# Performance work log

Measured on AMD Instinct MI355X. Metric: run time of the kernel, lower is better.

## Reference

```python
import jax, jax.numpy as jnp
import numpy as np

B, C, T, F = 8, 256, 256, 128
D, H, HEADS, K = 64, 128, 4, 8
I = D * K  # unfold channel dim = D*8


def _conv2d(x, w, b, stride=1, pad=0):
    y = jax.lax.conv_general_dilated(x, w, (stride, stride), [(pad, pad), (pad, pad)],
                                     dimension_numbers=('NCHW', 'OIHW', 'NCHW'))
    return y + b[None, :, None, None]


def _convT(x, w, b, strides):
    y = jax.lax.conv_transpose(x, w, strides, 'VALID', dimension_numbers=('NCHW', 'OIHW', 'NCHW'))
    return y + b[None, :, None, None]


def _sru_dir(x, Wx, bf, br, Whw):
    # x: (N, L, I). SRU: all matmuls precomputed, only elementwise recurrence in scan.
    u = jnp.einsum('nli,ih->nlh', x, Wx)  # (N, L, 3H)
    xt, fp, rp = jnp.split(u, 3, axis=-1)
    f = jax.nn.sigmoid(fp + bf)
    r = jax.nn.sigmoid(rp + br)
    xhw = jnp.einsum('nli,ih->nlh', x, Whw)  # highway projection (I != H)

    def step(c, inp):
        xt_t, f_t, r_t, xhw_t = inp
        c = f_t * c + (1.0 - f_t) * xt_t
        h = r_t * c + (1.0 - r_t) * xhw_t
        return c, h

    c0 = jnp.zeros((x.shape[0], bf.shape[-1]), x.dtype)
    seq = tuple(jnp.swapaxes(a, 0, 1) for a in (xt, f, r, xhw))  # (L, N, H)
    _, hs = jax.lax.scan(step, c0, seq)
    return jnp.swapaxes(hs, 0, 1)  # (N, L, H)


def _sru_bidir(x, Wx, bf, br, Whw):
    hf = _sru_dir(x, Wx[0], bf[0], br[0], Whw[0])
    hb = _sru_dir(x[:, ::-1], Wx[1], bf[1], br[1], Whw[1])[:, ::-1]
    return jnp.concatenate([hf, hb], axis=-1)  # (N, L, 2H)


def _unfold_last(x, k):
    # nn.Unfold(kernel=(1,k)) over last axis: (B,D,T,F) -> (B, D*k, T, F-k+1)
    L = x.shape[-1] - k + 1
    p = jnp.stack([x[..., i:i + L] for i in range(k)], axis=2)  # (B, D, k, T, L)
    b, d = x.shape[0], x.shape[1]
    return p.reshape(b, d * k, x.shape[2], L)


def _pathway(ag, Wx, bf, br, Whw, pw, pb, ctw, ctb):
    # unfold -> bidirectional SRU over last axis -> proj -> ConvTranspose2d(I->D, kernel (1,8))
    b, d, t, f = ag.shape
    L = f - K + 1
    u = _unfold_last(ag, K)                                  # (B, I, t, L)
    seq = u.transpose(0, 2, 3, 1).reshape(b * t, L, d * K)   # scan along unfolded axis
    h = _sru_bidir(seq, Wx, bf, br, Whw)                     # (b*t, L, 2H)
    z = h @ pw + pb                                          # (b*t, L, I)
    z = z.reshape(b, t, L, d * K).transpose(0, 3, 1, 2)      # (B, I, t, L)
    return _convT(z, ctw, ctb, (1, 1))                       # (B, D, t, f)


def _attention(x, qkv_w, qkv_b, ow, ob):
    b, d, t, f = x.shape
    n = t * f
    tok = x.reshape(b, d, n).transpose(0, 2, 1)  # (B, N, D)
    qkv = tok @ qkv_w + qkv_b
    q, k, v = jnp.split(qkv, 3, axis=-1)
    dh = d // HEADS
    sp = lambda a: a.reshape(b, n, HEADS, dh).transpose(0, 2, 1, 3)
    q, k, v = sp(q), sp(k), sp(v)
    s = jnp.einsum('bhnd,bhmd->bhnm', q, k) / jnp.sqrt(jnp.asarray(dh, x.dtype))
    a = jax.nn.softmax(s, axis=-1)
    o = jnp.einsum('bhnm,bhmd->bhnd', a, v).transpose(0, 2, 1, 3).reshape(b, n, d)
    o = o @ ow + ob
    return o.transpose(0, 2, 1).reshape(b, d, t, f)


def _forward(A, compress_w, compress_b, down_w0, down_b0, down_w1, down_b1,
             f_Wx, f_bf, f_br, f_Whw, f_proj_w, f_proj_b, f_ct_w, f_ct_b,
             t_Wx, t_bf, t_br, t_Whw, t_proj_w, t_proj_b, t_ct_w, t_ct_b,
             qkv_w, qkv_b, out_w, out_b, up_w0, up_b0, up_w1, up_b1, final_w, final_b):
    # Compressor: 1x1 conv C->D then 2 strided downsample units
    x0 = _conv2d(A, compress_w, compress_b)                              # (B,D,T,F)
    x1 = jax.nn.relu(_conv2d(x0, down_w0, down_b0, stride=2, pad=1))     # (B,D,T/2,F/2)
    x2 = jax.nn.relu(_conv2d(x1, down_w1, down_b1, stride=2, pad=1))     # (B,D,T/4,F/4)
    ag = x2
    # Dual path: frequency scan then time scan, with residuals as in _dual_path
    freq_out = _pathway(ag, f_Wx, f_bf, f_br, f_Whw, f_proj_w, f_proj_b, f_ct_w, f_ct_b) + ag
    agt = ag.transpose(0, 1, 3, 2)  # scan over time axis
    time_out = _pathway(agt, t_Wx, t_bf, t_br, t_Whw, t_proj_w, t_proj_b, t_ct_w, t_ct_b).transpose(0, 1, 3, 2) + freq_out
    # TF self-attention with residual
    dp = _attention(time_out, qkv_w, qkv_b, out_w, out_b) + time_out
    # U-Net style reconstruction with skips, project back to C
    y = _convT(dp, up_w0, up_b0, (2, 2)) + x1
    y = _convT(y, up_w1, up_b1, (2, 2)) + x0
    return _conv2d(y, final_w, final_b)                                  # (B,C,T,F)


def setup_inputs() -> dict:
    key = jax.random.key(0)
    ks = iter(jax.random.split(key, 64))

    def p(shape, scale=0.05):
        return jax.random.normal(next(ks), shape, dtype=jnp.float32) * scale

    inp = dict(
        A=jax.random.normal(next(ks), (B, C, T, F), dtype=jnp.float32),
        compress_w=p((D, C, 1, 1)), compress_b=p((D,)),
        down_w0=p((D, D, 3, 3)), down_b0=p((D,)),
        down_w1=p((D, D, 3, 3)), down_b1=p((D,)),
        f_Wx=p((2, I, 3 * H)), f_bf=p((2, H)), f_br=p((2, H)), f_Whw=p((2, I, H)),
        f_proj_w=p((2 * H, I)), f_proj_b=p((I,)), f_ct_w=p((D, I, 1, K)), f_ct_b=p((D,)),
        t_Wx=p((2, I, 3 * H)), t_bf=p((2, H)), t_br=p((2, H)), t_Whw=p((2, I, H)),
        t_proj_w=p((2 * H, I)), t_proj_b=p((I,)), t_ct_w=p((D, I, 1, K)), t_ct_b=p((D,)),
        qkv_w=p((D, 3 * D)), qkv_b=p((3 * D,)), out_w=p((D, D)), out_b=p((D,)),
        up_w0=p((D, D, 2, 2)), up_b0=p((D,)),
        up_w1=p((D, D, 2, 2)), up_b1=p((D,)),
        final_w=p((C, D, 1, 1)), final_b=p((C,)),
    )
    return inp


def reference(A, compress_w, compress_b, down_w0, down_b0, down_w1, down_b1,
              f_Wx, f_bf, f_br, f_Whw, f_proj_w, f_proj_b, f_ct_w, f_ct_b,
              t_Wx, t_bf, t_br, t_Whw, t_proj_w, t_proj_b, t_ct_w, t_ct_b,
              qkv_w, qkv_b, out_w, out_b, up_w0, up_b0, up_w1, up_b1, final_w, final_b):
    return _forward(A, compress_w, compress_b, down_w0, down_b0, down_w1, down_b1,
                    f_Wx, f_bf, f_br, f_Whw, f_proj_w, f_proj_b, f_ct_w, f_ct_b,
                    t_Wx, t_bf, t_br, t_Whw, t_proj_w, t_proj_b, t_ct_w, t_ct_b,
                    qkv_w, qkv_b, out_w, out_b, up_w0, up_b0, up_w1, up_b1, final_w, final_b)
```

## Files before the change

kernel.cpp:

```cpp
#include <hip/hip_runtime.h>

#define BB 8
#define CC 256
#define TT 256
#define FF 128
#define DD 64
#define HH 128
#define NHEADS 4
#define KK 8
#define II 512
#define T2 128
#define F2 64
#define T4 64
#define F4 32
#define P4 2048

#define LF 25
#define LT 57
#define MF (512*LF)
#define MT (256*LT)

typedef __attribute__((ext_vector_type(8))) short bf16x8;
typedef __attribute__((ext_vector_type(4))) float f32x4;

// ... 32 lines not shown
    if (bid < 64)        { int g = bid * 256 + tid; cw16[g] = f2b(cw[g]); return; }
    if (bid < 128)       { int g = (bid - 64) * 256 + tid; fw16[g] = f2b(fw[g]); return; }
    if (bid < 256) {
        const float* w = (bid < 192) ? upw0 : upw1;
        ushort* O = (bid < 192) ? WupT0 : WupT1;
        int g = ((bid - 128) & 63) * 256 + tid;
        int c = g & 63; int n = g >> 6;
        int parity = n >> 6, d = n & 63;
        O[g] = f2b(w[((d * 64 + c) * 2 + (1 - (parity >> 1))) * 2 + (1 - (parity & 1))]);
        return;
    }
    if (bid < 304) {
        int g = (bid - 256) * 256 + tid;
        int k = g & 63, n = g >> 6;
        qkvwT[g] = f2b(qkv_w[k * 192 + n]); return;
    }
    if (bid < 320) {
        int g = (bid - 304) * 256 + tid;
        int k = g & 63, n = g >> 6;
        owT[g] = f2b(ow[k * 64 + n]); return;
    }
    if (bid < 608) {
        const float* w = (bid < 464) ? dw0 : dw1;
        ushort* O = (bid < 464) ? WT9d0 : WT9d1;
        int g = ((bid - 320) % 144) * 256 + tid;
        int c = g & 63; int rest = g >> 6;
        int d = rest & 63; int tap = rest >> 6;
        O[g] = f2b(w[(d * 64 + c) * 9 + tap]); return;
    }
    if (bid < 1632) {
        const float* w = (bid < 1120) ? f_pw : t_pw;
        ushort* O = (bid < 1120) ? pwF16 : pwT16;
        int g = ((bid - 608) % 512) * 256 + tid;
        O[g] = f2b(w[g]); return;
    }
    if (bid < 3680) {
        const float* ctw = (bid < 2656) ? f_ctw : t_ctw;
        ushort* O = (bid < 2656) ? WctF : WctT_;
        int g = ((bid - 1632) % 1024) * 256 + tid;
        int k = g & 511; int n = g >> 9;
        int tap = n >> 6, d = n & 63;
        O[g] = f2b(ctw[((d * 512) + k) * 8 + tap]); return;
    }
    {
        const float* Wx  = (bid < 5728) ? f_Wx  : t_Wx;
        const float* Whw = (bid < 5728) ? f_Whw : t_Whw;
        ushort* O = (bid < 5728) ? WcatF : WcatTm;
        int g = ((bid - 3680) % 2048) * 256 + tid;
        int k = g & 511; int n = g >> 9;
        int dir = n >> 9; int c = n & 511;
        float v = (c < 384) ? Wx[(dir * 512 + k) * 384 + c]
                            : Whw[(dir * 512 + k) * 128 + (c - 384)];
        O[g] = f2b(v);
    }
}

__global__ __launch_bounds__(256) void w3_gemm_k(
    const ushort* __restrict__ pwA, const ushort* __restrict__ wctA,
    const ushort* __restrict__ pwB, const ushort* __restrict__ wctB,
    ushort* __restrict__ w3A, ushort* __restrict__ w3B)
{
    const int M = 256, K = 512;
    const ushort* A16  = blockIdx.z ? pwB  : pwA;
    const ushort* BT16 = blockIdx.z ? wctB : wctA;
    ushort* C16        = blockIdx.z ? w3B  : w3A;
    __shared__ ushort As[128][40];
    __shared__ ushort Bs[128][40];
    int m0 = blockIdx.y * 128, n0 = blockIdx.x * 128;
    int tid = threadIdx.x;
    int wave = tid >> 6, lane = tid & 63;
    int wm = (wave & 1) * 64, wn = (wave >> 1) * 64;
    int l15 = lane & 15, lhi = lane >> 4;
    f32x4 acc[4][4] = {};
    int rs = tid >> 2, qs = tid & 3;

    for (int k0 = 0; k0 < K; k0 += 32) {
        *(uint4*)&As[rs][qs * 8]      = *(const uint4*)(A16 + (long long)(m0 + rs) * K + k0 + qs * 8);
        *(uint4*)&As[rs + 64][qs * 8] = *(const uint4*)(A16 + (long long)(m0 + rs + 64) * K + k0 + qs * 8);
        *(uint4*)&Bs[rs][qs * 8]      = *(const uint4*)(BT16 + (long long)(n0 + rs) * K + k0 + qs * 8);
        *(uint4*)&Bs[rs + 64][qs * 8] = *(const uint4*)(BT16 + (long long)(n0 + rs + 64) * K + k0 + qs * 8);
        __syncthreads();
        bf16x8 af[4], bfr[4];
#pragma unroll
        for (int fr = 0; fr < 4; ++fr)
            af[fr] = *(const bf16x8*)&As[wm + fr * 16 + l15][lhi * 8];
#pragma unroll
        for (int fc = 0; fc < 4; ++fc)
            bfr[fc] = *(const bf16x8*)&Bs[wn + fc * 16 + l15][lhi * 8];
#pragma unroll
        for (int fr = 0; fr < 4; ++fr)
#pragma unroll
            for (int fc = 0; fc < 4; ++fc)
                acc[fr][fc] = __builtin_amdgcn_mfma_f32_16x16x32_bf16(af[fr], bfr[fc], acc[fr][fc], 0, 0, 0);
        __syncthreads();
    }
#pragma unroll
    for (int fr = 0; fr < 4; ++fr)
#pragma unroll
        for (int fc = 0; fc < 4; ++fc) {
            int col = n0 + wn + fc * 16 + l15;
#pragma unroll
            for (int r = 0; r < 4; ++r) {
                int row = m0 + wm + fr * 16 + lhi * 4 + r;
                C16[(long long)col * M + row] = f2b(acc[fr][fc][r]);
            }
        }
}

__global__ void bias3_red_k(const float* __restrict__ pbF, const float* __restrict__ ctwF,
                            const float* __restrict__ pbT, const float* __restrict__ ctwT,
                            float* __restrict__ b3F, float* __restrict__ b3T)
{
    int n = blockIdx.x; int path = blockIdx.y;
    const float* pb  = path ? pbT  : pbF;
    const float* ctw = path ? ctwT : ctwF;
    float* b3        = path ? b3T  : b3F;
    int d = n & 63, tap = n >> 6;
    int tid = threadIdx.x;
    float s = 0.f;
    for (int i = tid; i < 512; i += 256)
        s += pb[i] * ctw[(d * 512 + i) * 8 + tap];
    __shared__ float red[256];
    red[tid] = s; __syncthreads();
    for (int st = 128; st > 0; st >>= 1) {
        if (tid < st) red[tid] += red[tid + st];
        __syncthreads();
    }
    if (tid == 0) b3[n] = red[0];
}

__global__ void unfold_both_k(const float* __restrict__ ag,
                              ushort* __restrict__ uF, ushort* __restrict__ uT)
{
    long long gid = (long long)blockIdx.x * blockDim.x + threadIdx.x;
    if (gid < (long long)MF * II) {
        int ch = (int)(gid & 511); int row = (int)(gid >> 9);
        int b = row / (T4 * LF); int rem = row - b * (T4 * LF);
        int t = rem / LF; int l = rem - t * LF;
        int d = ch >> 3, i = ch & 7;
        uF[gid] = f2b(ag[((long long)((b * DD + d) * T4 + t)) * F4 + l + i]);
    } else {
        long long g2 = gid - (long long)MF * II;
        int ch = (int)(g2 & 511); int row = (int)(g2 >> 9);
        int b = row / (F4 * LT); int rem = row - b * (F4 * LT);
        int tt = rem / LT; int l = rem - tt * LT;
        int d = ch >> 3, i = ch & 7;
        uT[g2] = f2b(ag[((long long)((b * DD + d) * T4 + (l + i))) * F4 + tt]);
    }
}

__global__ __launch_bounds__(256) void gates_fused_k(
    const ushort* __restrict__ uF, const ushort* __restrict__ uT,
    const ushort* __restrict__ WF, const ushort* __restrict__ WTm,
    ushort* __restrict__ GxtF, ushort* __restrict__ GxhF,
    ushort* __restrict__ GfF, ushort* __restrict__ GrF,
    ushort* __restrict__ GxtT, ushort* __restrict__ GxhT,
    ushort* __restrict__ GfT, ushort* __restrict__ GrT,
    const float* __restrict__ f_bf, const float* __restrict__ f_br,
    const float* __restrict__ t_bf, const float* __restrict__ t_br)
{
    __shared__ ushort As[128][40];
    __shared__ ushort Bs[128][40];
    const int K = 512;
    int by = blockIdx.y;
    bool tp = by >= 100;
    const ushort* A16 = tp ? uT : uF;
    const ushort* WT  = tp ? WTm : WF;
    ushort* Gxt = tp ? GxtT : GxtF;
    ushort* Gxh = tp ? GxhT : GxhF;
    ushort* Gf = tp ? GfT : GfF;
    ushort* Gr = tp ? GrT : GrF;
    const float* bfw = tp ? t_bf : f_bf;
    const float* brw = tp ? t_br : f_br;
    int m0 = (tp ? by - 100 : by) * 128;
    int n0 = blockIdx.x * 128;
    int tid = threadIdx.x, wave = tid >> 6, lane = tid & 63;
    int wm = (wave & 1) * 64, wn = (wave >> 1) * 64;
    int l15 = lane & 15, lhi = lane >> 4;
    f32x4 acc[4][4] = {};
    int rs = tid >> 2, qs = tid & 3;

    for (int k0 = 0; k0 < K; k0 += 32) {
        *(uint4*)&As[rs][qs * 8]      = *(const uint4*)(A16 + (long long)(m0 + rs) * K + k0 + qs * 8);
        *(uint4*)&As[rs + 64][qs * 8] = *(const uint4*)(A16 + (long long)(m0 + rs + 64) * K + k0 + qs * 8);
        *(uint4*)&Bs[rs][qs * 8]      = *(const uint4*)(WT + (long long)(n0 + rs) * K + k0 + qs * 8);
        *(uint4*)&Bs[rs + 64][qs * 8] = *(const uint4*)(WT + (long long)(n0 + rs + 64) * K + k0 + qs * 8);
        __syncthreads();
        bf16x8 af[4], bfr[4];
#pragma unroll
        for (int fr = 0; fr < 4; ++fr)
            af[fr] = *(const bf16x8*)&As[wm + fr * 16 + l15][lhi * 8];
#pragma unroll
        for (int fc = 0; fc < 4; ++fc)
            bfr[fc] = *(const bf16x8*)&Bs[wn + fc * 16 + l15][lhi * 8];
#pragma unroll
        for (int fr = 0; fr < 4; ++fr)
#pragma unroll
            for (int fc = 0; fc < 4; ++fc)
                acc[fr][fc] = __builtin_amdgcn_mfma_f32_16x16x32_bf16(af[fr], bfr[fc], acc[fr][fc], 0, 0, 0);
        __syncthreads();
    }
#pragma unroll
    for (int fc = 0; fc < 4; ++fc) {
        int col = n0 + wn + fc * 16 + l15;
        int dir = col >> 9, c = col & 511;
        int cls = c >> 7, h = c & 127;
        int dh = dir * 128 + h;
#pragma unroll
        for (int fr = 0; fr < 4; ++fr) {
#pragma unroll
            for (int r = 0; r < 4; ++r) {
                int row = m0 + wm + fr * 16 + lhi * 4 + r;
                long long idx = (long long)row * 256 + dh;
                float v = acc[fr][fc][r];
                if (cls == 0)      Gxt[idx] = f2b(v);
                else if (cls == 3) Gxh[idx] = f2b(v);
                else if (cls == 1) Gf[idx] = f2b(1.f / (1.f + __expf(-(v + bfw[dh]))));
                else               Gr[idx] = f2b(1.f / (1.f + __expf(-(v + brw[dh]))));
            }
        }
    }
}

__global__ void sru_scan_both_k(
    const ushort* __restrict__ GxtF, const ushort* __restrict__ GxhF,
    const ushort* __restrict__ GfF, const ushort* __restrict__ GrF,
    ushort* __restrict__ hF,
    const ushort* __restrict__ GxtT, const ushort* __restrict__ GxhT,
    const ushort* __restrict__ GfT, const ushort* __restrict__ GrT,
    ushort* __restrict__ hT)
{
    int gid = blockIdx.x * blockDim.x + threadIdx.x;
    const ushort *Gxt, *Gxh, *Gf, *Gr; ushort* hout; int L;
    if (gid < 512 * 256) {
        Gxt = GxtF; Gxh = GxhF; Gf = GfF; Gr = GrF; hout = hF; L = LF;
    } else {
        gid -= 512 * 256;
        Gxt = GxtT; Gxh = GxhT; Gf = GfT; Gr = GrT; hout = hT; L = LT;
    }
    int h = gid & 127; int dir = (gid >> 7) & 1; int n = gid >> 8;
    int dh = dir * 128 + h;
    float c = 0.f;
    for (int s = 0; s < L; ++s) {
        int l = dir ? (L - 1 - s) : s;
        long long off = (long long)(n * L + l) * 256 + dh;
        float xt = b2f(Gxt[off]), xh = b2f(Gxh[off]);
        float f = b2f(Gf[off]);
        float r = b2f(Gr[off]);
        c = f * c + (1.f - f) * xt;
        float hv = r * c + (1.f - r) * xh;
        hout[off] = f2b(hv);
    }
}

__global__ __launch_bounds__(256) void gemmW_both_k(
    const ushort* __restrict__ hF, const ushort* __restrict__ W3F,
    ushort* __restrict__ YF, const float* __restrict__ b3F,
    const ushort* __restrict__ hT, const ushort* __restrict__ W3T,
    ushort* __restrict__ YT, const float* __restrict__ b3T)
{
    __shared__ ushort As[128][40];
    __shared__ ushort Bs[128][40];
    const int N = 512, K = 256;
    int by = blockIdx.y;
    bool tp = by >= 100;
    const ushort* A16 = tp ? hT : hF;
    const ushort* WT  = tp ? W3T : W3F;
    ushort* C16       = tp ? YT : YF;
    const float* bias = tp ? b3T : b3F;
    int m0 = (tp ? by - 100 : by) * 128;
    int n0 = blockIdx.x * 128;
    int tid = threadIdx.x, wave = tid >> 6, lane = tid & 63;
    int wm = (wave & 1) * 64, wn = (wave >> 1) * 64;
    int l15 = lane & 15, lhi = lane >> 4;
    f32x4 acc[4][4] = {};
    int rs = tid >> 2, qs = tid & 3;

    for (int k0 = 0; k0 < K; k0 += 32) {
        *(uint4*)&As[rs][qs * 8]      = *(const uint4*)(A16 + (long long)(m0 + rs) * K + k0 + qs * 8);
        *(uint4*)&As[rs + 64][qs * 8] = *(const uint4*)(A16 + (long long)(m0 + rs + 64) * K + k0 + qs * 8);
        *(uint4*)&Bs[rs][qs * 8]      = *(const uint4*)(WT + (long long)(n0 + rs) * K + k0 + qs * 8);
        *(uint4*)&Bs[rs + 64][qs * 8] = *(const uint4*)(WT + (long long)(n0 + rs + 64) * K + k0 + qs * 8);
        __syncthreads();
        bf16x8 af[4], bfr[4];
#pragma unroll
        for (int fr = 0; fr < 4; ++fr)
            af[fr] = *(const bf16x8*)&As[wm + fr * 16 + l15][lhi * 8];
#pragma unroll
        for (int fc = 0; fc < 4; ++fc)
            bfr[fc] = *(const bf16x8*)&Bs[wn + fc * 16 + l15][lhi * 8];
#pragma unroll
        for (int fr = 0; fr < 4; ++fr)
#pragma unroll
            for (int fc = 0; fc < 4; ++fc)
                acc[fr][fc] = __builtin_amdgcn_mfma_f32_16x16x32_bf16(af[fr], bfr[fc], acc[fr][fc], 0, 0, 0);
        __syncthreads();
    }
#pragma unroll
    for (int fc = 0; fc < 4; ++fc) {
        int col = n0 + wn + fc * 16 + l15;
        float bv = bias[col];
#pragma unroll
        for (int fr = 0; fr < 4; ++fr) {
#pragma unroll
            for (int r = 0; r < 4; ++r) {
                int row = m0 + wm + fr * 16 + lhi * 4 + r;
                C16[(long long)row * N + col] = f2b(acc[fr][fc][r] + bv);
            }
        }
    }
}

__global__ void dual_reduce_k(const ushort* __restrict__ YF, const ushort* __restrict__ YT,
                              const float* __restrict__ f_ctb, const float* __restrict__ t_ctb,
                              const float* __restrict__ ag, float* __restrict__ tout)
{
    int gid = blockIdx.x * blockDim.x + threadIdx.x;
    int d = gid & 63; int rest = gid >> 6;
    int f = rest & 31; rest >>= 5;
    int t = rest & 63; int b = rest >> 6;
    float v = f_ctb[d] + t_ctb[d];
    long long ybF = ((long long)(b * 64 + t)) * LF;
    long long ybT = ((long long)(b * 32 + f)) * LT;
#pragma unroll
    for (int tap = 0; tap < 8; ++tap) {
        int lf = f + tap - 7;
        if (lf >= 0 && lf < LF) v += b2f(YF[(ybF + lf) * 512 + tap * 64 + d]);
        int lt = t + tap - 7;
        if (lt >= 0 && lt < LT) v += b2f(YT[(ybT + lt) * 512 + tap * 64 + d]);
    }
    long long oi = (((long long)(b * 64 + d)) * 64 + t) * 32 + f;
    tout[oi] = v + ag[oi];
}

template<int BN>
__global__ __launch_bounds__(256) void mfma_nchw_k(
    const float* __restrict__ X, const ushort* __restrict__ WT,
    const float* __restrict__ bias, float* __restrict__ Y,
    int P, int N, int K)
{
    constexpr int FC = BN / 32;
    __shared__ ushort As[128][40];
    int p0 = blockIdx.x * 128;
    int n0 = blockIdx.y * BN;
    int b  = blockIdx.z;
    int tid = threadIdx.x, wave = tid >> 6, lane = tid & 63;
    int l15 = lane & 15, lhi = lane >> 4;
    int wm = (wave & 1) * 64, wn = (wave >> 1) * (BN / 2);
    f32x4 acc[4][FC] = {};
    const float* Xb = X + (long long)b * K * P;
    int kk_s = tid >> 3, pq_s = tid & 7;

    for (int k0 = 0; k0 < K; k0 += 32) {
        const float* xr = Xb + (long long)(k0 + kk_s) * P + p0;
#pragma unroll
        for (int j = 0; j < 4; ++j) {
            float4 v = *(const float4*)(xr + j * 32 + pq_s * 4);
            int pp = j * 32 + pq_s * 4;
            As[pp][kk_s]     = f2b(v.x);
            As[pp + 1][kk_s] = f2b(v.y);
            As[pp + 2][kk_s] = f2b(v.z);
            As[pp + 3][kk_s] = f2b(v.w);
        }
        __syncthreads();
        bf16x8 af[4], bfr[FC];
#pragma unroll
        for (int fr = 0; fr < 4; ++fr)
            af[fr] = *(const bf16x8*)&As[wm + fr * 16 + l15][lhi * 8];
#pragma unroll
        for (int fc = 0; fc < FC; ++fc)
            bfr[fc] = *(const bf16x8*)(WT + (long long)(n0 + wn + fc * 16 + l15) * K + k0 + lhi * 8);
#pragma unroll
        for (int fr = 0; fr < 4; ++fr)
#pragma unroll
            for (int fc = 0; fc < FC; ++fc)
                acc[fr][fc] = __builtin_amdgcn_mfma_f32_16x16x32_bf16(af[fr], bfr[fc], acc[fr][fc], 0, 0, 0);
        __syncthreads();
    }
#pragma unroll
    for (int fc = 0; fc < FC; ++fc) {
        int n = n0 + wn + fc * 16 + l15;
        float bv = bias[n];
        float* yr = Y + ((long long)(b * N + n)) * P + p0 + wm + lhi * 4;
#pragma unroll
        for (int fr = 0; fr < 4; ++fr) {
            float4 o;
            o.x = acc[fr][fc][0] + bv;
            o.y = acc[fr][fc][1] + bv;
            o.z = acc[fr][fc][2] + bv;
            o.w = acc[fr][fc][3] + bv;
            *(float4*)(yr + fr * 16) = o;
        }
    }
}

__global__ __launch_bounds__(256) void mfma_nchw16_k(
    const ushort* __restrict__ X, const ushort* __restrict__ WT,
    const float* __restrict__ bias, float* __restrict__ Y,
    int P, int N, int K)
{
    constexpr int BN = 128, FC = 4;
    __shared__ ushort As[128][40];
    int p0 = blockIdx.x * 128;
    int n0 = blockIdx.y * BN;
    int b  = blockIdx.z;
    int tid = threadIdx.x, wave = tid >> 6, lane = tid & 63;
    int l15 = lane & 15, lhi = lane >> 4;
    int wm = (wave & 1) * 64, wn = (wave >> 1) * (BN / 2);
    f32x4 acc[4][FC] = {};
    const ushort* Xb = X + (long long)b * K * P;
    int kk_s = tid >> 3, pq_s = tid & 7;

    for (int k0 = 0; k0 < K; k0 += 32) {
        const ushort* xr = Xb + (long long)(k0 + kk_s) * P + p0 + pq_s * 16;
#pragma unroll
        for (int j = 0; j < 2; ++j) {
            uint4 v = *(const uint4*)(xr + j * 8);
            const ushort* e = (const ushort*)&v;
            int pp = pq_s * 16 + j * 8;
#pragma unroll
            for (int t = 0; t < 8; ++t) As[pp + t][kk_s] = e[t];
        }
        __syncthreads();
        bf16x8 af[4], bfr[FC];
#pragma unroll
        for (int fr = 0; fr < 4; ++fr)
            af[fr] = *(const bf16x8*)&As[wm + fr * 16 + l15][lhi * 8];
#pragma unroll
        for (int fc = 0; fc < FC; ++fc)
            bfr[fc] = *(const bf16x8*)(WT + (long long)(n0 + wn + fc * 16 + l15) * K + k0 + lhi * 8);
#pragma unroll
        for (int fr = 0; fr < 4; ++fr)
#pragma unroll
            for (int fc = 0; fc < FC; ++fc)
                acc[fr][fc] = __builtin_amdgcn_mfma_f32_16x16x32_bf16(af[fr], bfr[fc], acc[fr][fc], 0, 0, 0);
        __syncthreads();
    }
#pragma unroll
    for (int fc = 0; fc < FC; ++fc) {
        int n = n0 + wn + fc * 16 + l15;
        float bv = bias[n];
        float* yr = Y + ((long long)(b * N + n)) * P + p0 + wm + lhi * 4;
#pragma unroll
        for (int fr = 0; fr < 4; ++fr) {
            float4 o;
            o.x = acc[fr][fc][0] + bv;
            o.y = acc[fr][fc][1] + bv;
            o.z = acc[fr][fc][2] + bv;
            o.w = acc[fr][fc][3] + bv;
            *(float4*)(yr + fr * 16) = o;
        }
    }
}

__global__ __launch_bounds__(256) void down_mfma_k(
    const float* __restrict__ in, const ushort* __restrict__ WT9,
    const float* __restrict__ bias, float* __restrict__ out,
    int Hi, int Wi)
{
    __shared__ ushort Is[289][64];
    int Ho = Hi >> 1, Wo = Wi >> 1;
    int ntx = Wo >> 3, nty = Ho >> 3;
    int tx = blockIdx.x % ntx; int rest = blockIdx.x / ntx;
    int ty = rest % nty; int b = rest / nty;
    int oy0 = ty * 8, ox0 = tx * 8;
    int iy0 = oy0 * 2 - 1, ix0 = ox0 * 2 - 1;
    int tid = threadIdx.x, wave = tid >> 6, lane = tid & 63;
    int l15 = lane & 15, lhi = lane >> 4;
    int wm = (wave & 1) * 32, wn = (wave >> 1) * 32;

    const float* ib = in + (long long)b * 64 * Hi * Wi;
    for (int i = tid; i < 289 * 64; i += 256) {
        int c = i / 289; int sp = i - c * 289;
        int r = sp / 17; int s = sp - r * 17;
        int iy = iy0 + r, ix = ix0 + s;
        float v = 0.f;
        if (iy >= 0 && iy < Hi && ix >= 0 && ix < Wi)
            v = ib[(long long)c * Hi * Wi + (long long)iy * Wi + ix];
        Is[sp][c ^ ((sp & 7) << 3)] = f2b(v);
    }
    __syncthreads();

    f32x4 acc[2][2] = {};
#pragma unroll
    for (int tap = 0; tap < 9; ++tap) {
        int kh = tap / 3, kw = tap - kh * 3;
#pragma unroll
        for (int half = 0; half < 2; ++half) {
            int c0 = half * 32 + lhi * 8;
            bf16x8 af[2], bw[2];
#pragma unroll
            for (int fr = 0; fr < 2; ++fr) {
                int p = wm + fr * 16 + l15;
                int sp = (2 * (p >> 3) + kh) * 17 + 2 * (p & 7) + kw;
                af[fr] = *(const bf16x8*)&Is[sp][c0 ^ ((sp & 7) << 3)];
            }
#pragma unroll
            for (int fc = 0; fc < 2; ++fc) {
                int d = wn + fc * 16 + l15;
                bw[fc] = *(const bf16x8*)(WT9 + (tap * 64 + d) * 64 + c0);
            }
#pragma unroll
            for (int fr = 0; fr < 2; ++fr)
#pragma unroll
                for (int fc = 0; fc < 2; ++fc)
                    acc[fr][fc] = __builtin_amdgcn_mfma_f32_16x16x32_bf16(af[fr], bw[fc], acc[fr][fc], 0, 0, 0);
        }
    }
#pragma unroll
    for (int fc = 0; fc < 2; ++fc) {
        int d = wn + fc * 16 + l15;
        float bv = bias[d];
        long long obase = ((long long)(b * 64 + d)) * Ho * Wo;
#pragma unroll
        for (int fr = 0; fr < 2; ++fr) {
#pragma unroll
            for (int r = 0; r < 4; ++r) {
                int p = wm + fr * 16 + lhi * 4 + r;
                int py = p >> 3, px = p & 7;
                out[obase + (long long)(oy0 + py) * Wo + ox0 + px] =
                    fmaxf(acc[fr][fc][r] + bv, 0.f);
            }
        }
    }
}

template<int OUT16>
__global__ __launch_bounds__(256) void up_mfma_k(
    const float* __restrict__ in, const ushort* __restrict__ WT,
    const float* __restrict__ bias, const float* __restrict__ resid,
    float* __restrict__ out, ushort* __restrict__ o16, int P, int wsh)
{
    __shared__ ushort As[128][72];
    int p0 = blockIdx.x * 128;
    int n0 = blockIdx.y * 128;
    int b  = blockIdx.z;
    int tid = threadIdx.x, wave = tid >> 6, lane = tid & 63;
    int l15 = lane & 15, lhi = lane >> 4;
    int wm = (wave & 1) * 64, wn = (wave >> 1) * 64;
    int Wi = 1 << wsh;
    int Ho = ((P >> wsh) << 1), Wo = Wi << 1;

    int kk_s = tid >> 3, pq_s = tid & 7;
#pragma unroll
    for (int h = 0; h < 2; ++h) {
        int k = h * 32 + kk_s;
        const float* xr = in + ((long long)(b * 64 + k)) * P + p0 + pq_s * 16;
#pragma unroll
        for (int j = 0; j < 4; ++j) {
            float4 v = *(const float4*)(xr + j * 4);
            int pp = pq_s * 16 + j * 4;
            As[pp][k]     = f2b(v.x);
            As[pp + 1][k] = f2b(v.y);
            As[pp + 2][k] = f2b(v.z);
            As[pp + 3][k] = f2b(v.w);
        }
    }
    __syncthreads();

    f32x4 acc[4][4] = {};
#pragma unroll
    for (int c = 0; c < 2; ++c) {
        bf16x8 af[4], bfr[4];
#pragma unroll
        for (int fr = 0; fr < 4; ++fr)
            af[fr] = *(const bf16x8*)&As[wm + fr * 16 + l15][c * 32 + lhi * 8];
#pragma unroll
        for (int fc = 0; fc < 4; ++fc)
            bfr[fc] = *(const bf16x8*)(WT + (long long)(n0 + wn + fc * 16 + l15) * 64 + c * 32 + lhi * 8);
#pragma unroll
        for (int fr = 0; fr < 4; ++fr)
#pragma unroll
            for (int fc = 0; fc < 4; ++fc)
                acc[fr][fc] = __builtin_amdgcn_mfma_f32_16x16x32_bf16(af[fr], bfr[fc], acc[fr][fc], 0, 0, 0);
    }

#pragma unroll
    for (int fc = 0; fc < 4; ++fc) {
        int n = n0 + wn + fc * 16 + l15;
        int parity = n >> 6, d = n & 63;
        int py = parity >> 1, px = parity & 1;
        float bv = bias[d];
        const long long obase = ((long long)(b * 64 + d)) * Ho * Wo;
#pragma unroll
        for (int fr = 0; fr < 4; ++fr) {
#pragma unroll
            for (int r = 0; r < 4; ++r) {
                int p = p0 + wm + fr * 16 + lhi * 4 + r;
                int iy = p >> wsh, ix = p & (Wi - 1);
                long long oi = obase + (long long)(2 * iy + py) * Wo + 2 * ix + px;
                float v = acc[fr][fc][r] + bv + resid[oi];
                if (OUT16) o16[oi] = f2b(v);
                else       out[oi] = v;
            }
        }
    }
}

__global__ __launch_bounds__(256) void mfma_qkv_k(
    const float* __restrict__ X, const ushort* __restrict__ WT,
    const float* __restrict__ bias, ushort* __restrict__ C16)
{
    __shared__ ushort As[128][72];
    int p0 = blockIdx.x * 128;
    int b  = blockIdx.z;
    int tid = threadIdx.x, wave = tid >> 6, lane = tid & 63;
    int l15 = lane & 15, lhi = lane >> 4;
    int wm = (wave & 1) * 64, wn = (wave >> 1) * 96;

    int kk_s = tid >> 3, pq_s = tid & 7;
#pragma unroll
    for (int h = 0; h < 2; ++h) {
        int k = h * 32 + kk_s;
        const float* xr = X + ((long long)(b * 64 + k)) * P4 + p0 + pq_s * 16;
#pragma unroll
        for (int j = 0; j < 4; ++j) {
            float4 v = *(const float4*)(xr + j * 4);
            int pp = pq_s * 16 + j * 4;
            As[pp][k]     = f2b(v.x);
            As[pp + 1][k] = f2b(v.y);
            As[pp + 2][k] = f2b(v.z);
            As[pp + 3][k] = f2b(v.w);
        }
    }
    __syncthreads();

    f32x4 acc[4][6] = {};
#pragma unroll
    for (int c = 0; c < 2; ++c) {
        bf16x8 af[4], bfr[6];
#pragma unroll
        for (int fr = 0; fr < 4; ++fr)
            af[fr] = *(const bf16x8*)&As[wm + fr * 16 + l15][c * 32 + lhi * 8];
#pragma unroll
        for (int fc = 0; fc < 6; ++fc)
            bfr[fc] = *(const bf16x8*)(WT + (long long)(wn + fc * 16 + l15) * 64 + c * 32 + lhi * 8);
#pragma unroll
        for (int fr = 0; fr < 4; ++fr)
#pragma unroll
            for (int fc = 0; fc < 6; ++fc)
                acc[fr][fc] = __builtin_amdgcn_mfma_f32_16x16x32_bf16(af[fr], bfr[fc], acc[fr][fc], 0, 0, 0);
    }
#pragma unroll
    for (int fc = 0; fc < 6; ++fc) {
        int n = wn + fc * 16 + l15;
        float bv = bias[n];
#pragma unroll
        for (int fr = 0; fr < 4; ++fr)
#pragma unroll
            for (int r = 0; r < 4; ++r) {
                int p = p0 + wm + fr * 16 + lhi * 4 + r;
                C16[((long long)(b * P4 + p)) * 192 + n] = f2b(acc[fr][fc][r] + bv);
            }
    }
}

__global__ __launch_bounds__(256) void mfma_attnout_k(
    const float* __restrict__ A, const ushort* __restrict__ owT,
    const float* __restrict__ ob, const float* __restrict__ resid,
    float* __restrict__ dp)
{
    __shared__ ushort As[128][72];
    int p0 = blockIdx.x * 128;
    int b  = blockIdx.z;
    int tid = threadIdx.x, wave = tid >> 6, lane = tid & 63;
    int l15 = lane & 15, lhi = lane >> 4;
    int wm = (wave & 1) * 64, wn = (wave >> 1) * 32;

    int rs = tid >> 2, qs = tid & 3;
#pragma unroll
    for (int h = 0; h < 2; ++h) {
        int row = h * 64 + rs;
        const float* ar = A + ((long long)(b * P4 + p0 + row)) * 64 + qs * 16;
#pragma unroll
        for (int j = 0; j < 4; ++j) {
            float4 v = *(const float4*)(ar + j * 4);
            int c = qs * 16 + j * 4;
            *(unsigned*)&As[row][c]     = cvtpk_bf16(v.x, v.y);
            *(unsigned*)&As[row][c + 2] = cvtpk_bf16(v.z, v.w);
        }
    }
    __syncthreads();

    f32x4 acc[4][2] = {};
#pragma unroll
    for (int c = 0; c < 2; ++c) {
        bf16x8 af[4], bfr[2];
#pragma unroll
        for (int fr = 0; fr < 4; ++fr)
            af[fr] = *(const bf16x8*)&As[wm + fr * 16 + l15][c * 32 + lhi * 8];
#pragma unroll
        for (int fc = 0; fc < 2; ++fc)
            bfr[fc] = *(const bf16x8*)(owT + (long long)(wn + fc * 16 + l15) * 64 + c * 32 + lhi * 8);
#pragma unroll
        for (int fr = 0; fr < 4; ++fr)
#pragma unroll
            for (int fc = 0; fc < 2; ++fc)
                acc[fr][fc] = __builtin_amdgcn_mfma_f32_16x16x32_bf16(af[fr], bfr[fc], acc[fr][fc], 0, 0, 0);
    }
#pragma unroll
    for (int fc = 0; fc < 2; ++fc) {
        int n = wn + fc * 16 + l15;
        float bv = ob[n];
        long long base = ((long long)(b * 64 + n)) * P4;
#pragma unroll
        for (int fr = 0; fr < 4; ++fr) {
            int p = p0 + wm + fr * 16 + lhi * 4;
            float4 rv = *(const float4*)(resid + base + p);
            float4 o;
            o.x = acc[fr][fc][0] + bv + rv.x;
            o.y = acc[fr][fc][1] + bv + rv.y;
            o.z = acc[fr][fc][2] + bv + rv.z;
            o.w = acc[fr][fc][3] + bv + rv.w;
            *(float4*)(dp + base + p) = o;
        }
    }
}

__global__ __launch_bounds__(256) void attn_mfma_k(const ushort* __restrict__ qkv,
                                                   float* __restrict__ out)
{
    __shared__ ushort Qs[128][40];
    __shared__ ushort Ks[64][40];
    __shared__ ushort VsT[16][72];
    __shared__ ushort Ps[128][72];
    int qt = blockIdx.x, h = blockIdx.y, b = blockIdx.z;
    int tid = threadIdx.x, wave = tid >> 6, lane = tid & 63;
    int l15 = lane & 15, lhi = lane >> 4;
    int q0 = wave * 32;

    for (int i = tid; i < 1024; i += 256) {
        int row = i >> 3, c = i & 7;
        *(unsigned*)&Qs[row][16 + c * 2] = 0u;
    }
    for (int i = tid; i < 512; i += 256) {
        int row = i >> 3, c = i & 7;
        *(unsigned*)&Ks[row][16 + c * 2] = 0u;
    }
    {
        const ushort* qp = qkv + ((long long)(b * P4 + qt * 128)) * 192 + h * 16;
        for (int i = tid; i < 2048; i += 256) {
            int row = i >> 4, d = i & 15;
            Qs[row][d] = f2b(b2f(qp[row * 192 + d]) * 0.25f);
        }
    }
    __syncthreads();

    float mmax[2] = {-1e30f, -1e30f};
    float lsum[2] = {0.f, 0.f};
    f32x4 oacc[2] = {};

    for (int k0 = 0; k0 < P4; k0 += 64) {
        const ushort* kp = qkv + ((long long)(b * P4 + k0)) * 192 + 64 + h * 16;
        for (int i = tid; i < 1024; i += 256) {
            int key = i >> 4, d = i & 15;
            Ks[key][d]  = kp[key * 192 + d];
            VsT[d][key] = kp[key * 192 + 64 + d];
        }
        __syncthreads();

        bf16x8 bq[2];
        bq[0] = *(const bf16x8*)&Qs[q0 + l15][lhi * 8];
        bq[1] = *(const bf16x8*)&Qs[q0 + 16 + l15][lhi * 8];
        f32x4 s[4][2];
#pragma unroll
        for (int fr = 0; fr < 4; ++fr) {
            bf16x8 ak = *(const bf16x8*)&Ks[fr * 16 + l15][lhi * 8];
            f32x4 z = {};
            s[fr][0] = __builtin_amdgcn_mfma_f32_16x16x32_bf16(ak, bq[0], z, 0, 0, 0);
            s[fr][1] = __builtin_amdgcn_mfma_f32_16x16x32_bf16(ak, bq[1], z, 0, 0, 0);
        }
#pragma unroll
        for (int fc = 0; fc < 2; ++fc) {
            float m = s[0][fc][0];
#pragma unroll
            for (int fr = 0; fr < 4; ++fr)
#pragma unroll
                for (int r = 0; r < 4; ++r) m = fmaxf(m, s[fr][fc][r]);
            m = fmaxf(m, __shfl_xor(m, 16));
            m = fmaxf(m, __shfl_xor(m, 32));
            float nm = fmaxf(mmax[fc], m);
            float corr = __expf(mmax[fc] - nm);
            mmax[fc] = nm;
            float ps = 0.f;
#pragma unroll
            for (int fr = 0; fr < 4; ++fr)
#pragma unroll
                for (int r = 0; r < 4; ++r) {
                    float p = __expf(s[fr][fc][r] - nm);
                    s[fr][fc][r] = p;
                    ps += p;
                }
            lsum[fc] = lsum[fc] * corr + ps;
#pragma unroll
            for (int r = 0; r < 4; ++r) oacc[fc][r] *= corr;
        }
#pragma unroll
        for (int fc = 0; fc < 2; ++fc)
#pragma unroll
            for (int fr = 0; fr < 4; ++fr) {
                uint2 pk;
                pk.x = cvtpk_bf16(s[fr][fc][0], s[fr][fc][1]);
                pk.y = cvtpk_bf16(s[fr][fc][2], s[fr][fc][3]);
                *(uint2*)&Ps[q0 + fc * 16 + l15][fr * 16 + lhi * 4] = pk;
            }
#pragma unroll
        for (int ks = 0; ks < 2; ++ks) {
            bf16x8 av = *(const bf16x8*)&VsT[l15][ks * 32 + lhi * 8];
#pragma unroll
            for (int fc = 0; fc < 2; ++fc) {
                bf16x8 bp = *(const bf16x8*)&Ps[q0 + fc * 16 + l15][ks * 32 + lhi * 8];
                oacc[fc] = __builtin_amdgcn_mfma_f32_16x16x32_bf16(av, bp, oacc[fc], 0, 0, 0);
            }
        }
        __syncthreads();
    }
#pragma unroll
    for (int fc = 0; fc < 2; ++fc) {
        float L = lsum[fc];
        L += __shfl_xor(L, 16);
        L += __shfl_xor(L, 32);
        float inv = 1.f / L;
        int q = qt * 128 + q0 + fc * 16 + l15;
        float* op = out + ((long long)(b * P4 + q)) * 64 + h * 16 + lhi * 4;
#pragma unroll
        for (int r = 0; r < 4; ++r) op[r] = oacc[fc][r] * inv;
    }
}

extern "C" void kernel_launch(void* const* d_in, const int* in_sizes, int n_in,
                              void* d_out, int out_size, void* d_ws, size_t ws_size,
                              hipStream_t stream)
{
    const float* A_in  = (const float*)d_in[0];
    const float* cw    = (const float*)d_in[1];
    const float* cb    = (const float*)d_in[2];
    const float* dw0   = (const float*)d_in[3];
    const float* db0   = (const float*)d_in[4];
    const float* dw1   = (const float*)d_in[5];
    const float* db1   = (const float*)d_in[6];
    const float* f_Wx  = (const float*)d_in[7];
    const float* f_bf  = (const float*)d_in[8];
    const float* f_br  = (const float*)d_in[9];
    const float* f_Whw = (const float*)d_in[10];
    const float* f_pw  = (const float*)d_in[11];
    const float* f_pb  = (const float*)d_in[12];
    const float* f_ctw = (const float*)d_in[13];
    const float* f_ctb = (const float*)d_in[14];
    const float* t_Wx  = (const float*)d_in[15];
    const float* t_bf  = (const float*)d_in[16];
    const float* t_br  = (const float*)d_in[17];
    const float* t_Whw = (const float*)d_in[18];
    const float* t_pw  = (const float*)d_in[19];
    const float* t_pb  = (const float*)d_in[20];
    const float* t_ctw = (const float*)d_in[21];
    const float* t_ctb = (const float*)d_in[22];
    const float* qkv_w = (const float*)d_in[23];
    const float* qkv_b = (const float*)d_in[24];
    const float* ow    = (const float*)d_in[25];
    const float* ob    = (const float*)d_in[26];
    const float* upw0  = (const float*)d_in[27];
    const float* upb0  = (const float*)d_in[28];
    const float* upw1  = (const float*)d_in[29];
    const float* upb1  = (const float*)d_in[30];
    const float* fw    = (const float*)d_in[31];
    const float* fb    = (const float*)d_in[32];

    float* ws  = (float*)d_ws;
    float* out = (float*)d_out;

    float* ag    = ws + 0;
    float* x1    = ws + 1048576;
    float* uFf   = ws + 5242880;
    float* uTf   = ws + 8519680;
    float* GxtF  = ws + 12255232;
    float* GxhF  = ws + 15532032;
    float* GxtT  = ws + 18808832;
    float* GxhT  = ws + 22544384;
    float* GfFf  = ws + 26279936;
    float* GrFf  = ws + 27918336;
    float* GfTf  = ws + 29556736;
    float* GrTf  = ws + 31424512;
    float* hFf   = ws + 33292288;
    float* hTf   = ws + 34930688;
    float* YF16f = ws + 5242880;
    float* YT16f = ws + 8519680;
    float* y016f = ws + 19267584;
    float* y1    = ws + 12255232;
    float* pwFf  = ws + 36798464;
    float* pwTf  = ws + 36864000;
    float* w3Ff  = ws + 36929536;
    float* w3Tf  = ws + 36995072;
    float* b3Ff  = ws + 37060608;
    float* b3Tf  = ws + 37061120;
    float* wctFf = ws + 37061632;
    float* wctTf = ws + 37192704;
    float* wcaFf = ws + 37323776;
    float* wcaTf = ws + 37585920;
    float* cw16f = ws + 37848064;
    float* fw16f = ws + 37856256;
    float* wup0f = ws + 37864448;
    float* wup1f = ws + 37872640;
    float* qkvwf = ws + 37880832;
    float* owtf  = ws + 37886976;
    float* wdw0f = ws + 37889024;
    float* wdw1f = ws + 37907456;
    float* tout  = ws + 37925888;
    float* qkvbf = ws + 38974464;
    float* attnO = ws + 40547328;
    float* dp    = ws + 41595904;

    ushort* uF     = (ushort*)uFf;
    ushort* uT     = (ushort*)uTf;
    ushort* GxtF16 = (ushort*)GxtF;
    ushort* GxhF16 = (ushort*)GxhF;
    ushort* GxtT16 = (ushort*)GxtT;
    ushort* GxhT16 = (ushort*)GxhT;
    ushort* GfF    = (ushort*)GfFf;
    ushort* GrF    = (ushort*)GrFf;
    ushort* GfT    = (ushort*)GfTf;
    ushort* GrT    = (ushort*)GrTf;
    ushort* hF     = (ushort*)hFf;
    ushort* hT     = (ushort*)hTf;
    ushort* YF16   = (ushort*)YF16f;
    ushort* YT16   = (ushort*)YT16f;
    ushort* y016   = (ushort*)y016f;
    ushort* pwF16  = (ushort*)pwFf;
    ushort* pwT16  = (ushort*)pwTf;
    ushort* W3F    = (ushort*)w3Ff;
    ushort* W3T_   = (ushort*)w3Tf;
    ushort* WctF   = (ushort*)wctFf;
    ushort* WctT_  = (ushort*)wctTf;
    ushort* WcatF  = (ushort*)wcaFf;
    ushort* WcatTm = (ushort*)wcaTf;
    ushort* qkv16  = (ushort*)qkvbf;
    ushort* cw16   = (ushort*)cw16f;
    ushort* fw16   = (ushort*)fw16f;
    ushort* WupT0  = (ushort*)wup0f;
    ushort* WupT1  = (ushort*)wup1f;
    ushort* qkvwT  = (ushort*)qkvwf;
    ushort* owT    = (ushort*)owtf;
    ushort* WT9d0  = (ushort*)wdw0f;
    ushort* WT9d1  = (ushort*)wdw1f;
    float*  x0     = out;

    dim3 blk(256);

    pack_all_k<<<dim3(7776), blk, 0, stream>>>(
        cw, fw, upw0, upw1, qkv_w, ow, dw0, dw1, f_pw, t_pw, f_ctw, t_ctw,
        f_Wx, f_Whw, t_Wx, t_Whw,
        cw16, fw16, WupT0, WupT1, qkvwT, owT, WT9d0, WT9d1,
        pwF16, pwT16, WctF, WctT_, WcatF, WcatTm);
    w3_gemm_k<<<dim3(4, 2, 2), blk, 0, stream>>>(pwF16, WctF, pwT16, WctT_, W3F, W3T_);
    bias3_red_k<<<dim3(512, 2), blk, 0, stream>>>(f_pb, f_ctw, t_pb, t_ctw, b3Ff, b3Tf);

    mfma_nchw_k<64><<<dim3(256, 1, 8), blk, 0, stream>>>(A_in, cw16, cb, x0, 32768, 64, 256);

    down_mfma_k<<<dim3(1024), blk, 0, stream>>>(x0, WT9d0, db0, x1, TT, FF);
    down_mfma_k<<<dim3(256), blk, 0, stream>>>(x1, WT9d1, db1, ag, T2, F2);

    unfold_both_k<<<dim3(54784), blk, 0, stream>>>(ag, uF, uT);
    gates_fused_k<<<dim3(8, 214), blk, 0, stream>>>(uF, uT, WcatF, WcatTm,
        GxtF16, GxhF16, GfF, GrF, GxtT16, GxhT16, GfT, GrT, f_bf, f_br, t_bf, t_br);
    sru_scan_both_k<<<dim3(768), blk, 0, stream>>>(GxtF16, GxhF16, GfF, GrF, hF,
                                                   GxtT16, GxhT16, GfT, GrT, hT);
    gemmW_both_k<<<dim3(4, 214), blk, 0, stream>>>(hF, W3F, YF16, b3Ff,
                                                   hT, W3T_, YT16, b3Tf);
    dual_reduce_k<<<dim3(8192), blk, 0, stream>>>(YF16, YT16, f_ctb, t_ctb, ag, tout);

    mfma_qkv_k<<<dim3(16, 1, 8), blk, 0, stream>>>(tout, qkvwT, qkv_b, qkv16);
    attn_mfma_k<<<dim3(16, NHEADS, BB), blk, 0, stream>>>(qkv16, attnO);
    mfma_attnout_k<<<dim3(16, 1, 8), blk, 0, stream>>>(attnO, owT, ob, tout, dp);

    up_mfma_k<0><<<dim3(16, 2, 8), blk, 0, stream>>>(dp, WupT0, upb0, x1, y1, nullptr, 2048, 5);
    up_mfma_k<1><<<dim3(64, 2, 8), blk, 0, stream>>>(y1, WupT1, upb1, x0, nullptr, y016, 8192, 6);

    mfma_nchw16_k<<<dim3(256, 2, 8), blk, 0, stream>>>(y016, fw16, fb, out, 32768, 256, 64);
}
```

Before: 680.2 us.

## Store encoder activations in bf16 and keep SRU xt/highway gates in fp32

The compress conv output and the first downsample output are now stored as bf16 and reused as bf16 residuals in the upsampling path, which halves their read/write traffic. The SRU candidate and highway projections are instead written as fp32 rather than bf16, presumably for accuracy, which doubles that traffic. The workspace is re-laid out with aliased buffers to fit the new sizes. The change trades activation bandwidth against precision in the residual path.

```diff
diff --git a/kernel.cpp b/kernel.cpp
--- a/kernel.cpp
+++ b/kernel.cpp
@@ -208,9 +208,9 @@
 __global__ __launch_bounds__(256) void gates_fused_k(
     const ushort* __restrict__ uF, const ushort* __restrict__ uT,
     const ushort* __restrict__ WF, const ushort* __restrict__ WTm,
-    ushort* __restrict__ GxtF, ushort* __restrict__ GxhF,
+    float* __restrict__ GxtF, float* __restrict__ GxhF,
     ushort* __restrict__ GfF, ushort* __restrict__ GrF,
-    ushort* __restrict__ GxtT, ushort* __restrict__ GxhT,
+    float* __restrict__ GxtT, float* __restrict__ GxhT,
     ushort* __restrict__ GfT, ushort* __restrict__ GrT,
     const float* __restrict__ f_bf, const float* __restrict__ f_br,
     const float* __restrict__ t_bf, const float* __restrict__ t_br)
@@ -222,8 +222,8 @@
     bool tp = by >= 100;
     const ushort* A16 = tp ? uT : uF;
     const ushort* WT  = tp ? WTm : WF;
-    ushort* Gxt = tp ? GxtT : GxtF;
-    ushort* Gxh = tp ? GxhT : GxhF;
+    float* Gxt = tp ? GxtT : GxtF;
+    float* Gxh = tp ? GxhT : GxhF;
     ushort* Gf = tp ? GfT : GfF;
     ushort* Gr = tp ? GrT : GrF;
     const float* bfw = tp ? t_bf : f_bf;
@@ -269,8 +269,8 @@
                 int row = m0 + wm + fr * 16 + lhi * 4 + r;
                 long long idx = (long long)row * 256 + dh;
                 float v = acc[fr][fc][r];
-                if (cls == 0)      Gxt[idx] = f2b(v);
-                else if (cls == 3) Gxh[idx] = f2b(v);
+                if (cls == 0)      Gxt[idx] = v;
+                else if (cls == 3) Gxh[idx] = v;
                 else if (cls == 1) Gf[idx] = f2b(1.f / (1.f + __expf(-(v + bfw[dh]))));
                 else               Gr[idx] = f2b(1.f / (1.f + __expf(-(v + brw[dh]))));
             }
@@ -279,15 +279,15 @@
 }
 
 __global__ void sru_scan_both_k(
-    const ushort* __restrict__ GxtF, const ushort* __restrict__ GxhF,
+    const float* __restrict__ GxtF, const float* __restrict__ GxhF,
     const ushort* __restrict__ GfF, const ushort* __restrict__ GrF,
     ushort* __restrict__ hF,
-    const ushort* __restrict__ GxtT, const ushort* __restrict__ GxhT,
+    const float* __restrict__ GxtT, const float* __restrict__ GxhT,
     const ushort* __restrict__ GfT, const ushort* __restrict__ GrT,
     ushort* __restrict__ hT)
 {
     int gid = blockIdx.x * blockDim.x + threadIdx.x;
-    const ushort *Gxt, *Gxh, *Gf, *Gr; ushort* hout; int L;
+    const float *Gxt, *Gxh; const ushort *Gf, *Gr; ushort* hout; int L;
     if (gid < 512 * 256) {
         Gxt = GxtF; Gxh = GxhF; Gf = GfF; Gr = GrF; hout = hF; L = LF;
     } else {
@@ -300,7 +300,7 @@
     for (int s = 0; s < L; ++s) {
         int l = dir ? (L - 1 - s) : s;
         long long off = (long long)(n * L + l) * 256 + dh;
-        float xt = b2f(Gxt[off]), xh = b2f(Gxh[off]);
+        float xt = Gxt[off], xh = Gxh[off];
         float f = b2f(Gf[off]);
         float r = b2f(Gr[off]);
         c = f * c + (1.f - f) * xt;
@@ -389,20 +389,19 @@
     tout[oi] = v + ag[oi];
 }
 
-template<int BN>
-__global__ __launch_bounds__(256) void mfma_nchw_k(
+__global__ __launch_bounds__(256) void mfma_nchw_o16_k(
     const float* __restrict__ X, const ushort* __restrict__ WT,
-    const float* __restrict__ bias, float* __restrict__ Y,
+    const float* __restrict__ bias, ushort* __restrict__ Y16,
     int P, int N, int K)
 {
-    constexpr int FC = BN / 32;
+    constexpr int FC = 2;
     __shared__ ushort As[128][40];
     int p0 = blockIdx.x * 128;
-    int n0 = blockIdx.y * BN;
+    int n0 = 0;
     int b  = blockIdx.z;
     int tid = threadIdx.x, wave = tid >> 6, lane = tid & 63;
     int l15 = lane & 15, lhi = lane >> 4;
-    int wm = (wave & 1) * 64, wn = (wave >> 1) * (BN / 2);
+    int wm = (wave & 1) * 64, wn = (wave >> 1) * 32;
     f32x4 acc[4][FC] = {};
     const float* Xb = X + (long long)b * K * P;
     int kk_s = tid >> 3, pq_s = tid & 7;
@@ -437,15 +436,13 @@
     for (int fc = 0; fc < FC; ++fc) {
         int n = n0 + wn + fc * 16 + l15;
         float bv = bias[n];
-        float* yr = Y + ((long long)(b * N + n)) * P + p0 + wm + lhi * 4;
+        ushort* yr = Y16 + ((long long)(b * N + n)) * P + p0 + wm + lhi * 4;
 #pragma unroll
         for (int fr = 0; fr < 4; ++fr) {
-            float4 o;
-            o.x = acc[fr][fc][0] + bv;
-            o.y = acc[fr][fc][1] + bv;
-            o.z = acc[fr][fc][2] + bv;
-            o.w = acc[fr][fc][3] + bv;
-            *(float4*)(yr + fr * 16) = o;
+            uint2 o;
+            o.x = cvtpk_bf16(acc[fr][fc][0] + bv, acc[fr][fc][1] + bv);
+            o.y = cvtpk_bf16(acc[fr][fc][2] + bv, acc[fr][fc][3] + bv);
+            *(uint2*)(yr + fr * 16) = o;
         }
     }
 }
@@ -509,10 +506,11 @@
     }
 }
 
+template<int OUT16>
 __global__ __launch_bounds__(256) void down_mfma_k(
-    const float* __restrict__ in, const ushort* __restrict__ WT9,
+    const ushort* __restrict__ in, const ushort* __restrict__ WT9,
     const float* __restrict__ bias, float* __restrict__ out,
-    int Hi, int Wi)
+    ushort* __restrict__ o16, int Hi, int Wi)
 {
     __shared__ ushort Is[289][64];
     int Ho = Hi >> 1, Wo = Wi >> 1;
@@ -525,15 +523,15 @@
     int l15 = lane & 15, lhi = lane >> 4;
     int wm = (wave & 1) * 32, wn = (wave >> 1) * 32;
 
-    const float* ib = in + (long long)b * 64 * Hi * Wi;
+    const ushort* ib = in + (long long)b * 64 * Hi * Wi;
     for (int i = tid; i < 289 * 64; i += 256) {
         int c = i / 289; int sp = i - c * 289;
         int r = sp / 17; int s = sp - r * 17;
         int iy = iy0 + r, ix = ix0 + s;
-        float v = 0.f;
+        ushort v = 0;
         if (iy >= 0 && iy < Hi && ix >= 0 && ix < Wi)
             v = ib[(long long)c * Hi * Wi + (long long)iy * Wi + ix];
-        Is[sp][c ^ ((sp & 7) << 3)] = f2b(v);
+        Is[sp][c ^ ((sp & 7) << 3)] = v;
     }
     __syncthreads();
 
@@ -574,8 +572,10 @@
             for (int r = 0; r < 4; ++r) {
                 int p = wm + fr * 16 + lhi * 4 + r;
                 int py = p >> 3, px = p & 7;
-                out[obase + (long long)(oy0 + py) * Wo + ox0 + px] =
-                    fmaxf(acc[fr][fc][r] + bv, 0.f);
+                long long oi = obase + (long long)(oy0 + py) * Wo + ox0 + px;
+                float v = fmaxf(acc[fr][fc][r] + bv, 0.f);
+                if (OUT16) o16[oi] = f2b(v);
+                else       out[oi] = v;
             }
         }
     }
@@ -584,7 +584,7 @@
 template<int OUT16>
 __global__ __launch_bounds__(256) void up_mfma_k(
     const float* __restrict__ in, const ushort* __restrict__ WT,
-    const float* __restrict__ bias, const float* __restrict__ resid,
+    const float* __restrict__ bias, const ushort* __restrict__ resid16,
     float* __restrict__ out, ushort* __restrict__ o16, int P, int wsh)
 {
     __shared__ ushort As[128][72];
@@ -645,7 +645,7 @@
                 int p = p0 + wm + fr * 16 + lhi * 4 + r;
                 int iy = p >> wsh, ix = p & (Wi - 1);
                 long long oi = obase + (long long)(2 * iy + py) * Wo + 2 * ix + px;
-                float v = acc[fr][fc][r] + bv + resid[oi];
+                float v = acc[fr][fc][r] + bv + b2f(resid16[oi]);
                 if (OUT16) o16[oi] = f2b(v);
                 else       out[oi] = v;
             }
@@ -926,52 +926,51 @@
     float* out = (float*)d_out;
 
     float* ag    = ws + 0;
-    float* x1    = ws + 1048576;
-    float* uFf   = ws + 5242880;
-    float* uTf   = ws + 8519680;
-    float* GxtF  = ws + 12255232;
-    float* GxhF  = ws + 15532032;
-    float* GxtT  = ws + 18808832;
-    float* GxhT  = ws + 22544384;
-    float* GfFf  = ws + 26279936;
-    float* GrFf  = ws + 27918336;
-    float* GfTf  = ws + 29556736;
-    float* GrTf  = ws + 31424512;
-    float* hFf   = ws + 33292288;
-    float* hTf   = ws + 34930688;
-    float* YF16f = ws + 5242880;
-    float* YT16f = ws + 8519680;
-    float* y016f = ws + 19267584;
-    float* y1    = ws + 12255232;
-    float* pwFf  = ws + 36798464;
-    float* pwTf  = ws + 36864000;
-    float* w3Ff  = ws + 36929536;
-    float* w3Tf  = ws + 36995072;
-    float* b3Ff  = ws + 37060608;
-    float* b3Tf  = ws + 37061120;
-    float* wctFf = ws + 37061632;
-    float* wctTf = ws + 37192704;
-    float* wcaFf = ws + 37323776;
-    float* wcaTf = ws + 37585920;
-    float* cw16f = ws + 37848064;
-    float* fw16f = ws + 37856256;
-    float* wup0f = ws + 37864448;
-    float* wup1f = ws + 37872640;
-    float* qkvwf = ws + 37880832;
-    float* owtf  = ws + 37886976;
-    float* wdw0f = ws + 37889024;
-    float* wdw1f = ws + 37907456;
-    float* tout  = ws + 37925888;
-    float* qkvbf = ws + 38974464;
-    float* attnO = ws + 40547328;
-    float* dp    = ws + 41595904;
-
+    float* x016f = ws + 1048576;
+    float* x116f = ws + 9437184;
+    float* uFf   = ws + 11534336;
+    float* uTf   = ws + 14811136;
+    float* GxtF  = ws + 18546688;
+    float* GxhF  = ws + 21823488;
+    float* GxtT  = ws + 25100288;
+    float* GxhT  = ws + 28835840;
+    float* GfFf  = ws + 32571392;
+    float* GrFf  = ws + 34209792;
+    float* GfTf  = ws + 35848192;
+    float* GrTf  = ws + 37715968;
+    float* hFf   = ws + 39583744;
+    float* hTf   = ws + 41222144;
+    float* YF16f = uFf;
+    float* YT16f = uTf;
+    float* y1    = GxtF;
+    float* y016f = GxtT;
+    float* tout  = hFf;
+    float* dp    = hTf;
+    float* qkvbf = uFf;
+    float* attnO = uTf;
+    float* pwFf  = ws + 43089920;
+    float* pwTf  = ws + 43155456;
+    float* w3Ff  = ws + 43220992;
+    float* w3Tf  = ws + 43286528;
+    float* b3Ff  = ws + 43352064;
+    float* b3Tf  = ws + 43352576;
+    float* wctFf = ws + 43353088;
+    float* wctTf = ws + 43484160;
+    float* wcaFf = ws + 43615232;
+    float* wcaTf = ws + 43877376;
+    float* cw16f = ws + 44139520;
+    float* fw16f = ws + 44147712;
+    float* wup0f = ws + 44155904;
+    float* wup1f = ws + 44164096;
+    float* qkvwf = ws + 44172288;
+    float* owtf  = ws + 44178432;
+    float* wdw0f = ws + 44180480;
+    float* wdw1f = ws + 44198912;
+
+    ushort* x016   = (ushort*)x016f;
+    ushort* x116   = (ushort*)x116f;
     ushort* uF     = (ushort*)uFf;
     ushort* uT     = (ushort*)uTf;
-    ushort* GxtF16 = (ushort*)GxtF;
-    ushort* GxhF16 = (ushort*)GxhF;
-    ushort* GxtT16 = (ushort*)GxtT;
-    ushort* GxhT16 = (ushort*)GxhT;
     ushort* GfF    = (ushort*)GfFf;
     ushort* GrF    = (ushort*)GrFf;
     ushort* GfT    = (ushort*)GfTf;
@@ -981,6 +980,7 @@
     ushort* YF16   = (ushort*)YF16f;
     ushort* YT16   = (ushort*)YT16f;
     ushort* y016   = (ushort*)y016f;
+    ushort* qkv16  = (ushort*)qkvbf;
     ushort* pwF16  = (ushort*)pwFf;
     ushort* pwT16  = (ushort*)pwTf;
     ushort* W3F    = (ushort*)w3Ff;
@@ -989,7 +989,6 @@
     ushort* WctT_  = (ushort*)wctTf;
     ushort* WcatF  = (ushort*)wcaFf;
     ushort* WcatTm = (ushort*)wcaTf;
-    ushort* qkv16  = (ushort*)qkvbf;
     ushort* cw16   = (ushort*)cw16f;
     ushort* fw16   = (ushort*)fw16f;
     ushort* WupT0  = (ushort*)wup0f;
@@ -998,7 +997,6 @@
     ushort* owT    = (ushort*)owtf;
     ushort* WT9d0  = (ushort*)wdw0f;
     ushort* WT9d1  = (ushort*)wdw1f;
-    float*  x0     = out;
 
     dim3 blk(256);
 
@@ -1010,16 +1008,16 @@
     w3_gemm_k<<<dim3(4, 2, 2), blk, 0, stream>>>(pwF16, WctF, pwT16, WctT_, W3F, W3T_);
     bias3_red_k<<<dim3(512, 2), blk, 0, stream>>>(f_pb, f_ctw, t_pb, t_ctw, b3Ff, b3Tf);
 
-    mfma_nchw_k<64><<<dim3(256, 1, 8), blk, 0, stream>>>(A_in, cw16, cb, x0, 32768, 64, 256);
-
-    down_mfma_k<<<dim3(1024), blk, 0, stream>>>(x0, WT9d0, db0, x1, TT, FF);
-    down_mfma_k<<<dim3(256), blk, 0, stream>>>(x1, WT9d1, db1, ag, T2, F2);
+    mfma_nchw_o16_k<<<dim3(256, 1, 8), blk, 0, stream>>>(A_in, cw16, cb, x016, 32768, 64, 256);
+
+    down_mfma_k<1><<<dim3(1024), blk, 0, stream>>>(x016, WT9d0, db0, nullptr, x116, TT, FF);
+    down_mfma_k<0><<<dim3(256), blk, 0, stream>>>(x116, WT9d1, db1, ag, nullptr, T2, F2);
 
     unfold_both_k<<<dim3(54784), blk, 0, stream>>>(ag, uF, uT);
     gates_fused_k<<<dim3(8, 214), blk, 0, stream>>>(uF, uT, WcatF, WcatTm,
-        GxtF16, GxhF16, GfF, GrF, GxtT16, GxhT16, GfT, GrT, f_bf, f_br, t_bf, t_br);
-    sru_scan_both_k<<<dim3(768), blk, 0, stream>>>(GxtF16, GxhF16, GfF, GrF, hF,
-                                                   GxtT16, GxhT16, GfT, GrT, hT);
+        GxtF, GxhF, GfF, GrF, GxtT, GxhT, GfT, GrT, f_bf, f_br, t_bf, t_br);
+    sru_scan_both_k<<<dim3(768), blk, 0, stream>>>(GxtF, GxhF, GfF, GrF, hF,
+                                                   GxtT, GxhT, GfT, GrT, hT);
     gemmW_both_k<<<dim3(4, 214), blk, 0, stream>>>(hF, W3F, YF16, b3Ff,
                                                    hT, W3T_, YT16, b3Tf);
     dual_reduce_k<<<dim3(8192), blk, 0, stream>>>(YF16, YT16, f_ctb, t_ctb, ag, tout);
@@ -1028,8 +1026,8 @@
     attn_mfma_k<<<dim3(16, NHEADS, BB), blk, 0, stream>>>(qkv16, attnO);
     mfma_attnout_k<<<dim3(16, 1, 8), blk, 0, stream>>>(attnO, owT, ob, tout, dp);
 
-    up_mfma_k<0><<<dim3(16, 2, 8), blk, 0, stream>>>(dp, WupT0, upb0, x1, y1, nullptr, 2048, 5);
-    up_mfma_k<1><<<dim3(64, 2, 8), blk, 0, stream>>>(y1, WupT1, upb1, x0, nullptr, y016, 8192, 6);
+    up_mfma_k<0><<<dim3(16, 2, 8), blk, 0, stream>>>(dp, WupT0, upb0, x116, y1, nullptr, 2048, 5);
+    up_mfma_k<1><<<dim3(64, 2, 8), blk, 0, stream>>>(y1, WupT1, upb1, x016, nullptr, y016, 8192, 6);
 
     mfma_nchw16_k<<<dim3(256, 2, 8), blk, 0, stream>>>(y016, fw16, fb, out, 32768, 256, 64);
 }
```

After: 671.1 us. About the same (-1.3%).
